# Kernel tuning notes

Measured on AMD Instinct MI355X. Metric: run time of the kernel, lower is better.

## Reference

```python
import jax, jax.numpy as jnp
import numpy as np

E, H, V, P, RAW = 512, 1024, 12000, 36, 2048
B, L = 128, 21

def setup_inputs() -> dict:
    key = jax.random.key(0)
    ks = jax.random.split(key, 16)
    n = lambda k, sh: (0.02 * jax.random.normal(k, sh)).astype(jnp.float32)
    z = lambda sh: jnp.zeros(sh, jnp.float32)
    return {
        "images_features": jax.random.normal(ks[0], (B, P, RAW), dtype=jnp.float32),
        "encoded_captions": jax.random.randint(ks[1], (B, L), 0, V),
        "caption_lengths": L,
        "W_img": n(ks[2], (RAW, H)), "b_img": z((H,)),
        "W_glob": n(ks[3], (H, E)), "b_glob": z((E,)),
        "W_ih1": n(ks[4], (2 * E + H, 4 * H)), "W_hh1": n(ks[5], (H, 4 * H)),
        "b_ih1": z((4 * H,)), "b_hh1": z((4 * H,)),
        "Wx_gate": n(ks[6], (2 * E + H, H)), "bx_gate": z((H,)),
        "Wh_gate": n(ks[7], (H, H)), "bh_gate": z((H,)),
        "W_ih2": n(ks[8], (2 * H, 4 * H)), "W_hh2": n(ks[9], (H, 4 * H)),
        "b_ih2": z((4 * H,)), "b_hh2": z((4 * H,)),
        "Wv": n(ks[10], (H, P)), "bv": z((P,)),
        "Ws": n(ks[11], (H, P)), "bs": z((P,)),
        "Wg": n(ks[12], (H, P)),
        "wh": n(ks[13], (P,)),
        "emb": n(ks[14], (V, E)),
        "W_fc": n(ks[15], (H, V)), "b_fc": z((V,)),
    }

def _lstm(x, h, c, W_ih, W_hh, b_ih, b_hh):
    # torch LSTMCell gate order: i, f, g, o
    g = x @ W_ih + b_ih + h @ W_hh + b_hh
    i, f, gg, o = jnp.split(g, 4, axis=-1)
    c_new = jax.nn.sigmoid(f) * c + jax.nn.sigmoid(i) * jnp.tanh(gg)
    h_new = jax.nn.sigmoid(o) * jnp.tanh(c_new)
    return h_new, c_new

def reference(images_features, encoded_captions, caption_lengths, W_img, b_img,
              W_glob, b_glob, W_ih1, W_hh1, b_ih1, b_hh1, Wx_gate, bx_gate,
              Wh_gate, bh_gate, W_ih2, W_hh2, b_ih2, b_hh2, Wv, bv, Ws, bs,
              Wg, wh, emb, W_fc, b_fc):
    Bsz = images_features.shape[0]
    Hd = W_hh1.shape[0]
    T = int(caption_lengths) - 1
    Vfeat = jax.nn.relu(images_features @ W_img + b_img)            # (B,P,H)
    glob = jax.nn.relu(jnp.mean(Vfeat, axis=1) @ W_glob + b_glob)   # (B,E)
    img_proj = Vfeat @ Wv + bv                                      # (B,P,P) loop-invariant
    word_embs = emb[encoded_captions[:, :T]]                        # (B,T,E)

    def step(carry, we):
        h1, c1, h2, c2 = carry
        xt = jnp.concatenate([h2, glob, we], axis=-1)               # (B, H+2E)
        h1n, c1n = _lstm(xt, h1, c1, W_ih1, W_hh1, b_ih1, b_hh1)
        sen_gate = jax.nn.sigmoid(xt @ Wx_gate + bx_gate + h1 @ Wh_gate + bh_gate)
        st = sen_gate * jnp.tanh(c1n)                               # visual sentinel
        ht_proj = h1n @ Wg                                          # (B,P)
        z = jnp.tanh(img_proj + ht_proj[:, :, None]) @ wh           # (B,P)
        alpha = jax.nn.softmax(z, axis=1)                           # (B,P)
        context = jnp.einsum('bp,bph->bh', alpha, Vfeat)            # (B,H)
        att_vs = jnp.tanh(st @ Ws + bs + ht_proj) @ wh              # (B,)
        alpha_hat = jax.nn.softmax(jnp.concatenate([z, att_vs[:, None]], axis=1), axis=1)
        beta = alpha_hat[:, -1:]                                    # (B,1)
        c_hat = beta * st + (1.0 - beta) * context
        h2n, c2n = _lstm(jnp.concatenate([c_hat, h1n], axis=-1), h2, c2,
                         W_ih2, W_hh2, b_ih2, b_hh2)
        score = (c_hat + h2n) @ W_fc + b_fc                         # (B,V)
        return (h1n, c1n, h2n, c2n), (score, alpha, beta)

    zeros = jnp.zeros((Bsz, Hd), images_features.dtype)
    init = (zeros, zeros, zeros, zeros)
    _, (preds, alphas, betas) = jax.lax.scan(step, init, jnp.swapaxes(word_embs, 0, 1))
    return (jnp.swapaxes(preds, 0, 1),   # (B,T,V)
            jnp.swapaxes(alphas, 0, 1),  # (B,T,P)
            jnp.swapaxes(betas, 0, 1))   # (B,T,1)
```

## Files before the change

kernel.cpp:

```cpp
#include <hip/hip_runtime.h>
#include <hip/hip_bf16.h>
#include <math.h>

typedef __attribute__((ext_vector_type(4))) float f32x4;
typedef __attribute__((ext_vector_type(8))) short bf16x8;

constexpr int kB = 128, kT = 20, kH = 1024, kE = 512, kP = 36, kRaw = 2048, kV = 12000;

__device__ __forceinline__ float sigf(float x) { return 1.0f / (1.0f + expf(-x)); }

#define AS1C const __attribute__((address_space(1))) void*
#define AS3P __attribute__((address_space(3))) void*

constexpr int NZ1 = 2 * kB * kH / 4;
constexpr int NZ2 = 2 * kB * kH * 2 / 16;
constexpr int NCV = kB * kP * kRaw / 4;
constexpr int NPV = 64 * 1024 * 2 / 16;
constexpr int NPF = 32 * 1024 * 2 / 16;
constexpr int NPB = 5120;
constexpr int NGE = kB * kT * kE;

__global__ __launch_bounds__(256) void prep_small(
    float* c1z, uint4* h1z, const float* images, __hip_bfloat16* imagesb,
    uint4* wtv, uint4* wtfc_pad,
    const float* b_ih1, const float* b_hh1, const float* bx, const float* bh,
    const float* b_ih2, const float* b_hh2, float* bias_g1, float* bias_g2,
    const int* caps, const float* emb, __hip_bfloat16* wembb) {
  long idx = (long)blockIdx.x * 256 + threadIdx.x;
  if (idx < NZ1) { reinterpret_cast<float4*>(c1z)[idx] = make_float4(0, 0, 0, 0); return; }
  idx -= NZ1;
  if (idx < NZ2) { h1z[idx] = make_uint4(0, 0, 0, 0); return; }
  idx -= NZ2;
  if (idx < NCV) {
    float4 v = reinterpret_cast<const float4*>(images)[idx];
    __hip_bfloat16* d = imagesb + idx * 4;
    d[0] = __float2bfloat16(v.x); d[1] = __float2bfloat16(v.y);
    d[2] = __float2bfloat16(v.z); d[3] = __float2bfloat16(v.w);
    return;
  }
  idx -= NCV;
  if (idx < NPV) { wtv[idx] = make_uint4(0, 0, 0, 0); return; }
  idx -= NPV;
  if (idx < NPF) { wtfc_pad[idx] = make_uint4(0, 0, 0, 0); return; }
  idx -= NPF;
  if (idx < NPB) {
    int i = (int)idx;
    if (i < 4096) {
      bias_g1[i] = b_ih1[i] + b_hh1[i];
      bias_g2[i] = b_ih2[i] + b_hh2[i];
    } else {
      bias_g1[i] = bx[i - 4096] + bh[i - 4096];
    }
    return;
  }
  idx -= NPB;
  if (idx < NGE) {
    int e = (int)(idx % kE);
    int bt = (int)(idx / kE);
    int t = bt % kT;
    int b = bt / kT;
    int tok = caps[b * (kT + 1) + t];
    wembb[idx] = __float2bfloat16(emb[(size_t)tok * kE + e]);
  }
}

struct TJob {
  const float* src; __hip_bfloat16* dst;
  int ld_src, K, N, lddst, koff, noff, blk_off, nbx;
};
struct TAll { TJob job[11]; int njobs; int total_blocks; };

__global__ __launch_bounds__(256) void transpose_all(TAll ta) {
  __shared__ float t[32][33];
  int bid = blockIdx.x;
  int ji = 0;
  while (ji + 1 < ta.njobs && bid >= ta.job[ji + 1].blk_off) ++ji;
  const TJob& J = ta.job[ji];
  int lbid = bid - J.blk_off;
  int n0 = (lbid % J.nbx) * 32, k0 = (lbid / J.nbx) * 32;
  int tx = threadIdx.x & 31, ty = threadIdx.x >> 5;
  #pragma unroll
  for (int i = 0; i < 32; i += 8) {
    int k = k0 + ty + i, n = n0 + tx;
    t[ty + i][tx] = (k < J.K && n < J.N) ? J.src[(size_t)k * J.ld_src + n] : 0.0f;
  }
  __syncthreads();
  #pragma unroll
  for (int i = 0; i < 32; i += 8) {
    int n = n0 + ty + i, k = k0 + tx;
    if (n < J.N && k < J.K)
      J.dst[(size_t)(n + J.noff) * J.lddst + k + J.koff] = __float2bfloat16(t[tx][ty + i]);
  }
}

struct SegB { const __hip_bfloat16* A; int lda; int kstart; int kend; };
struct GemmBArgs {
  SegB seg[4]; int nseg;
  const __hip_bfloat16* WT; int ldk;
  const float* bias;
  float* C; __hip_bfloat16* C16; int ldc; int N; int Ktot; int act; int zstride;
};

__global__ __launch_bounds__(256) void gemm_bf16(GemmBArgs ga) {
  __shared__ char lds[65536];
  const int bm = blockIdx.y * 64;
  const int bn = blockIdx.x * 64;
  const int tid = threadIdx.x;
  const int lane = tid & 63;
  const int w = tid >> 6;
  const int wr = w >> 1, wc = w & 1;

  int rowS[4], scbS[4], dstS[4];
  #pragma unroll
  for (int j = 0; j < 4; ++j) {
    int off = ((j * 4 + w) * 64 + lane) * 16;
    int row = off >> 8, colb = off & 255;
    rowS[j] = row;
    scbS[j] = colb ^ ((row & 7) << 4);
    dstS[j] = (j * 4 + w) * 1024;
  }

  f32x4 acc[2][2] = {};
  const int nz = gridDim.z;
  const int nit = (ga.Ktot >> 7) / nz;
  const int it0 = blockIdx.z * nit;
  float* C = ga.C + (size_t)blockIdx.z * ga.zstride;

  auto stage = [&](int it, int buf) {
    const int k0 = it << 7;
    int si = 0;
    while (k0 >= ga.seg[si].kend) ++si;
    const __hip_bfloat16* Aseg = ga.seg[si].A;
    const int lda = ga.seg[si].lda;
    const int ks = k0 - ga.seg[si].kstart;
    char* baseA = lds + buf * 32768;
    char* baseB = baseA + 16384;
    #pragma unroll
    for (int j = 0; j < 4; ++j) {
      const __hip_bfloat16* sA = Aseg + (size_t)(bm + rowS[j]) * lda + ks + (scbS[j] >> 1);
      __builtin_amdgcn_global_load_lds((AS1C)sA, (AS3P)(baseA + dstS[j]), 16, 0, 0);
      const __hip_bfloat16* sB = ga.WT + (size_t)(bn + rowS[j]) * ga.ldk + k0 + (scbS[j] >> 1);
      __builtin_amdgcn_global_load_lds((AS1C)sB, (AS3P)(baseB + dstS[j]), 16, 0, 0);
    }
  };

  auto compute = [&](int buf) {
    const char* baseA = lds + buf * 32768;
    const char* baseB = baseA + 16384;
    #pragma unroll
    for (int kk = 0; kk < 4; ++kk) {
      bf16x8 a[2], b[2];
      #pragma unroll
      for (int f = 0; f < 2; ++f) {
        int row = wr * 32 + f * 16 + (lane & 15);
        int cb = kk * 64 + (lane >> 4) * 16;
        a[f] = *(const bf16x8*)(baseA + row * 256 + (cb ^ ((row & 7) << 4)));
        int nl = wc * 32 + f * 16 + (lane & 15);
        b[f] = *(const bf16x8*)(baseB + nl * 256 + (cb ^ ((nl & 7) << 4)));
      }
      #pragma unroll
      for (int fm = 0; fm < 2; ++fm)
        #pragma unroll
        for (int fn = 0; fn < 2; ++fn)
          acc[fm][fn] = __builtin_amdgcn_mfma_f32_16x16x32_bf16(a[fm], b[fn], acc[fm][fn], 0, 0, 0);
    }
  };

  stage(it0, 0);
  stage(it0 + 1, 1);
  asm volatile("s_waitcnt vmcnt(8)" ::: "memory");
  __builtin_amdgcn_s_barrier();
  int cur = 0;
  for (int i = 0; i < nit; ++i) {
    compute(cur);
    __builtin_amdgcn_s_barrier();
    if (i + 2 < nit) stage(it0 + i + 2, cur);
    if (i + 1 < nit) {
      if (i + 2 < nit) asm volatile("s_waitcnt vmcnt(8)" ::: "memory");
      else             asm volatile("s_waitcnt vmcnt(0)" ::: "memory");
      __builtin_amdgcn_s_barrier();
    }
    cur ^= 1;
  }

  #pragma unroll
  for (int fm = 0; fm < 2; ++fm) {
    int rbase = bm + wr * 32 + fm * 16 + (lane >> 4) * 4;
    #pragma unroll
    for (int fn = 0; fn < 2; ++fn) {
      int col = bn + wc * 32 + fn * 16 + (lane & 15);
      if (col >= ga.N) continue;
      float bv = ga.bias ? ga.bias[col] : 0.0f;
      #pragma unroll
      for (int j = 0; j < 4; ++j) {
        float v = acc[fm][fn][j] + bv;
        if (ga.act == 1) v = fmaxf(v, 0.0f);
        size_t off = (size_t)(rbase + j) * ga.ldc + col;
        if (ga.C) C[off] = v;
        if (ga.C16) ga.C16[off] = __float2bfloat16(v);
      }
    }
  }
}

struct G128Args {
  const __hip_bfloat16* A; int lda;
  const __hip_bfloat16* WT; int ldk;
  const float* bias;
  float* C; __hip_bfloat16* C16; int ldc; int N; int Ktot; int act; int cmap;
};

__global__ __launch_bounds__(256) void gemm128(G128Args ga) {
  __shared__ char lds[65536];
  const int gx = gridDim.x;
  const int nwg = gx * gridDim.y;
  int bid = blockIdx.y * gx + blockIdx.x;
  int q = nwg >> 3, r = nwg & 7;
  int xc = bid & 7, yq = bid >> 3;
  int swz = (xc < r ? xc * (q + 1) : r * (q + 1) + (xc - r) * q) + yq;
  const int bn = (swz % gx) * 128;
  const int bm = (swz / gx) * 128;

  const int tid = threadIdx.x;
  const int lane = tid & 63;
  const int w = tid >> 6;
  const int wr = w >> 1, wc = w & 1;

  int rowS[4], scbS[4], dstS[4];
  #pragma unroll
  for (int j = 0; j < 4; ++j) {
    int off = ((j * 4 + w) * 64 + lane) * 16;
    int row = off >> 7, colb = off & 127;
    rowS[j] = row;
    scbS[j] = colb ^ ((row & 7) << 4);
    dstS[j] = (j * 4 + w) * 1024;
  }

  f32x4 acc[4][4] = {};
  const int nit = ga.Ktot >> 6;

  auto stage = [&](int it, int buf) {
    const int k0 = it << 6;
    char* baseA = lds + buf * 32768;
    char* baseB = baseA + 16384;
    #pragma unroll
    for (int j = 0; j < 4; ++j) {
      const __hip_bfloat16* sA = ga.A + (size_t)(bm + rowS[j]) * ga.lda + k0 + (scbS[j] >> 1);
      __builtin_amdgcn_global_load_lds((AS1C)sA, (AS3P)(baseA + dstS[j]), 16, 0, 0);
      const __hip_bfloat16* sB = ga.WT + (size_t)(bn + rowS[j]) * ga.ldk + k0 + (scbS[j] >> 1);
      __builtin_amdgcn_global_load_lds((AS1C)sB, (AS3P)(baseB + dstS[j]), 16, 0, 0);
    }
  };

  auto compute = [&](int buf) {
    const char* baseA = lds + buf * 32768;
    const char* baseB = baseA + 16384;
    #pragma unroll
    for (int kk = 0; kk < 2; ++kk) {
      bf16x8 a[4], b[4];
      int cb = kk * 64 + (lane >> 4) * 16;
      #pragma unroll
      for (int f = 0; f < 4; ++f) {
        int row = wr * 64 + f * 16 + (lane & 15);
        a[f] = *(const bf16x8*)(baseA + row * 128 + (cb ^ ((row & 7) << 4)));
        int nl = wc * 64 + f * 16 + (lane & 15);
        b[f] = *(const bf16x8*)(baseB + nl * 128 + (cb ^ ((nl & 7) << 4)));
      }
      #pragma unroll
      for (int fm = 0; fm < 4; ++fm)
        #pragma unroll
        for (int fn = 0; fn < 4; ++fn)
          acc[fm][fn] = __builtin_amdgcn_mfma_f32_16x16x32_bf16(a[fm], b[fn], acc[fm][fn], 0, 0, 0);
    }
  };

  stage(0, 0);
  stage(1, 1);
  asm volatile("s_waitcnt vmcnt(8)" ::: "memory");
  __builtin_amdgcn_s_barrier();
  int cur = 0;
  for (int i = 0; i < nit; ++i) {
    compute(cur);
    __builtin_amdgcn_s_barrier();
    if (i + 2 < nit) stage(i + 2, cur);
    if (i + 1 < nit) {
      if (i + 2 < nit) asm volatile("s_waitcnt vmcnt(8)" ::: "memory");
      else             asm volatile("s_waitcnt vmcnt(0)" ::: "memory");
      __builtin_amdgcn_s_barrier();
    }
    cur ^= 1;
  }

  #pragma unroll
  for (int fm = 0; fm < 4; ++fm) {
    int rbase = bm + wr * 64 + fm * 16 + (lane >> 4) * 4;
    #pragma unroll
    for (int fn = 0; fn < 4; ++fn) {
      int col = bn + wc * 64 + fn * 16 + (lane & 15);
      if (col >= ga.N) continue;
      float bv = ga.bias ? ga.bias[col] : 0.0f;
      #pragma unroll
      for (int j = 0; j < 4; ++j) {
        float v = acc[fm][fn][j] + bv;
        if (ga.act == 1) v = fmaxf(v, 0.0f);
        int m = rbase + j;
        size_t off = ga.cmap == 1
            ? (size_t)(m & 127) * ga.ldc + (size_t)(m >> 7) * kV + col
            : (size_t)m * ga.ldc + col;
        if (ga.C) ga.C[off] = v;
        if (ga.C16) ga.C16[off] = __float2bfloat16(v);
      }
    }
  }
}

__global__ __launch_bounds__(256) void mean_p(const float* __restrict__ Vfeat,
                                              __hip_bfloat16* __restrict__ meanVb) {
  int idx = blockIdx.x * 256 + threadIdx.x;
  if (idx >= kB * kH) return;
  int b = idx >> 10, h = idx & 1023;
  float sm = 0.0f;
  for (int p = 0; p < kP; ++p) sm += Vfeat[((size_t)b * kP + p) * kH + h];
  meanVb[idx] = __float2bfloat16(sm * (1.0f / kP));
}

constexpr int kSlab1 = kB * 5120;
__global__ __launch_bounds__(256) void step1_fused(
    const float* __restrict__ g, const float* __restrict__ bias_g1,
    float* __restrict__ c1, __hip_bfloat16* __restrict__ h1b,
    const float* __restrict__ img_proj, const float* __restrict__ Vfeat,
    const float* __restrict__ Wg, const float* __restrict__ Ws,
    const float* __restrict__ bs, const float* __restrict__ wh,
    float* __restrict__ c_hat, __hip_bfloat16* __restrict__ c_hatb,
    float* __restrict__ out_alphas, float* __restrict__ out_betas, int t) {
  const int b = blockIdx.x;
  const int tid = threadIdx.x;
  const int lane = tid & 63;
  const int w = tid >> 6;
  __shared__ float sh_h1[kH];
  __shared__ float sh_st[kH];
  __shared__ float wsum[4][36];
  __shared__ float htp[36];
  __shared__ float stp[36];
  __shared__ float alpha[kP];
  __shared__ float sred[4];

  const float* gr0 = g + (size_t)b * 5120;
  const float* gr1 = gr0 + kSlab1;
  #pragma unroll
  for (int i = 0; i < 4; ++i) {
    int h = tid + i * 256;
    float ig = sigf(gr0[h]           + gr1[h]           + bias_g1[h]);
    float fg = sigf(gr0[kH + h]      + gr1[kH + h]      + bias_g1[kH + h]);
    float gg = tanhf(gr0[2 * kH + h] + gr1[2 * kH + h]  + bias_g1[2 * kH + h]);
    float og = sigf(gr0[3 * kH + h]  + gr1[3 * kH + h]  + bias_g1[3 * kH + h]);
    int idx = b * kH + h;
    float c = fg * c1[idx] + ig * gg;
    float tc = tanhf(c);
    float hn = og * tc;
    c1[idx] = c;
    h1b[idx] = __float2bfloat16(hn);
    sh_h1[h] = hn;
    sh_st[h] = sigf(gr0[4 * kH + h] + gr1[4 * kH + h] + bias_g1[4 * kH + h]) * tc;
  }
  __syncthreads();

  #pragma unroll
  for (int pass = 0; pass < 2; ++pass) {
    const float* vec = pass == 0 ? sh_h1 : sh_st;
    const float* W = pass == 0 ? Wg : Ws;
    float pg[36];
    #pragma unroll
    for (int j = 0; j < 36; ++j) pg[j] = 0.0f;
    #pragma unroll
    for (int i = 0; i < 4; ++i) {
      int hh = tid + i * 256;
      float hv = vec[hh];
      const float4* wrow = reinterpret_cast<const float4*>(W + (size_t)hh * 36);
      #pragma unroll
      for (int r = 0; r < 9; ++r) {
        float4 wv = wrow[r];
        pg[4 * r + 0] = fmaf(hv, wv.x, pg[4 * r + 0]);
        pg[4 * r + 1] = fmaf(hv, wv.y, pg[4 * r + 1]);
        pg[4 * r + 2] = fmaf(hv, wv.z, pg[4 * r + 2]);
        pg[4 * r + 3] = fmaf(hv, wv.w, pg[4 * r + 3]);
      }
    }
    #pragma unroll
    for (int j = 0; j < 36; ++j) {
      float v = pg[j];
      #pragma unroll
      for (int off = 32; off > 0; off >>= 1) v += __shfl_down(v, off, 64);
      if (lane == 0) wsum[w][j] = v;
    }
    __syncthreads();
    if (tid < 36) {
      float s = wsum[0][tid] + wsum[1][tid] + wsum[2][tid] + wsum[3][tid];
      if (pass == 0) htp[tid] = s; else stp[tid] = s;
    }
    __syncthreads();
  }

  if (w == 0) {
    float zz_r = -3.0e38f;
    if (lane < kP) {
      const float* ip = img_proj + ((size_t)b * kP + lane) * kP;
      float acc = 0.0f;
      #pragma unroll
      for (int j = 0; j < kP; ++j) acc = fmaf(tanhf(ip[j] + htp[j]), wh[j], acc);
      zz_r = acc;
    }
    float m = zz_r;
    #pragma unroll
    for (int off = 32; off > 0; off >>= 1) m = fmaxf(m, __shfl_xor(m, off, 64));
    float e = (lane < kP) ? expf(zz_r - m) : 0.0f;
    float s = e;
    #pragma unroll
    for (int off = 32; off > 0; off >>= 1) s += __shfl_xor(s, off, 64);
    if (lane < kP) alpha[lane] = e / s;
    if (lane == 0) { sred[2] = m; sred[3] = s; }
  } else if (w == 1) {
    float tv = 0.0f;
    if (lane < kP) tv = tanhf(stp[lane] + bs[lane] + htp[lane]) * wh[lane];
    #pragma unroll
    for (int off = 32; off > 0; off >>= 1) tv += __shfl_xor(tv, off, 64);
    if (lane == 0) sred[0] = tv;
  }
  __syncthreads();
  if (tid == 0) {
    float av = sred[0], m = sred[2], s = sred[3];
    float m2 = fmaxf(m, av);
    float eb = expf(av - m2);
    float beta = eb / (s * expf(m - m2) + eb);
    sred[1] = beta;
    out_betas[b * kT + t] = beta;
  }
  __syncthreads();
  if (tid < kP) out_alphas[((size_t)b * kT + t) * kP + tid] = alpha[tid];
  const float beta = sred[1];
  #pragma unroll
  for (int i = 0; i < 4; ++i) {
    int h = tid + i * 256;
    float ctx = 0.0f;
    for (int p = 0; p < kP; ++p) ctx = fmaf(alpha[p], Vfeat[((size_t)b * kP + p) * kH + h], ctx);
    float v = beta * sh_st[h] + (1.0f - beta) * ctx;
    c_hat[(size_t)b * kH + h] = v;
    c_hatb[(size_t)b * kH + h] = __float2bfloat16(v);
  }
}

constexpr int kSlab2 = kB * 4096;
__global__ __launch_bounds__(256) void lstm2_elem(const float* __restrict__ g,
                                                  const float* __restrict__ bias_g2,
                                                  float* __restrict__ c2,
                                                  __hip_bfloat16* __restrict__ h2b,
                                                  const float* __restrict__ c_hat,
                                                  __hip_bfloat16* __restrict__ sbufb) {
  int idx = blockIdx.x * 256 + threadIdx.x;
  if (idx >= kB * kH) return;
  int b = idx >> 10, h = idx & 1023;
  const float* gr0 = g + (size_t)b * 4 * kH;
  const float* gr1 = gr0 + kSlab2;
  float ig = sigf(gr0[h]           + gr1[h]           + bias_g2[h]);
  float fg = sigf(gr0[kH + h]      + gr1[kH + h]      + bias_g2[kH + h]);
  float gg = tanhf(gr0[2 * kH + h] + gr1[2 * kH + h]  + bias_g2[2 * kH + h]);
  float og = sigf(gr0[3 * kH + h]  + gr1[3 * kH + h]  + bias_g2[3 * kH + h]);
  float c = fg * c2[idx] + ig * gg;
  float hn = og * tanhf(c);
  c2[idx] = c;
  h2b[idx] = __float2bfloat16(hn);
  sbufb[idx] = __float2bfloat16(c_hat[idx] + hn);
}

extern "C" void kernel_launch(void* const* d_in, const int* in_sizes, int n_in,
                              void* d_out, int out_size, void* d_ws, size_t ws_size,
                              hipStream_t stream) {
  const float* images  = (const float*)d_in[0];
  const int*   caps    = (const int*)d_in[1];
  const float* W_img   = (const float*)d_in[3];
  const float* b_img   = (const float*)d_in[4];
  const float* W_glob  = (const float*)d_in[5];
  const float* b_glob  = (const float*)d_in[6];
  const float* W_ih1   = (const float*)d_in[7];
  const float* W_hh1   = (const float*)d_in[8];
  const float* b_ih1   = (const float*)d_in[9];
  const float* b_hh1   = (const float*)d_in[10];
  const float* Wx_gate = (const float*)d_in[11];
  const float* bx_gate = (const float*)d_in[12];
  const float* Wh_gate = (const float*)d_in[13];
  const float* bh_gate = (const float*)d_in[14];
  const float* W_ih2   = (const float*)d_in[15];
  const float* W_hh2   = (const float*)d_in[16];
  const float* b_ih2   = (const float*)d_in[17];
  const float* b_hh2   = (const float*)d_in[18];
  const float* Wv      = (const float*)d_in[19];
  const float* bv      = (const float*)d_in[20];
  const float* Ws_     = (const float*)d_in[21];
  const float* bs_     = (const float*)d_in[22];
  const float* Wg      = (const float*)d_in[23];
  const float* wh      = (const float*)d_in[24];
  const float* emb     = (const float*)d_in[25];
  const float* W_fc    = (const float*)d_in[26];
  const float* b_fc    = (const float*)d_in[27];

  float* out = (float*)d_out;
  float* out_alphas = out + (size_t)kB * kT * kV;
  float* out_betas  = out_alphas + (size_t)kB * kT * kP;

  char* base = (char*)d_ws;
  auto alloc = [&](size_t bytes) {
    char* p = base;
    base += (bytes + 255) & ~(size_t)255;
    return p;
  };
  float*          Vfeat   = (float*)alloc((size_t)kB * kP * kH * 4);
  __hip_bfloat16* Vfeatb  = (__hip_bfloat16*)alloc((size_t)kB * kP * kH * 2);
  __hip_bfloat16* imagesb = (__hip_bfloat16*)alloc((size_t)kB * kP * kRaw * 2);
  __hip_bfloat16* WTg1    = (__hip_bfloat16*)alloc((size_t)5120 * 3072 * 2);
  __hip_bfloat16* WTg2    = (__hip_bfloat16*)alloc((size_t)4096 * 3072 * 2);
  __hip_bfloat16* WTfc    = (__hip_bfloat16*)alloc((size_t)12032 * 1024 * 2);
  __hip_bfloat16* WTimg   = (__hip_bfloat16*)alloc((size_t)1024 * 2048 * 2);
  __hip_bfloat16* WTglob  = (__hip_bfloat16*)alloc((size_t)512 * 1024 * 2);
  __hip_bfloat16* WTv     = (__hip_bfloat16*)alloc((size_t)64 * 1024 * 2);
  __hip_bfloat16* wembb   = (__hip_bfloat16*)alloc((size_t)kB * kT * kE * 2);
  float*          img_proj= (float*)alloc((size_t)kB * kP * kP * 4);
  __hip_bfloat16* globb   = (__hip_bfloat16*)alloc((size_t)kB * kE * 2);
  __hip_bfloat16* meanVb  = (__hip_bfloat16*)alloc((size_t)kB * kH * 2);
  float*          c1      = (float*)alloc((size_t)2 * kB * kH * 4);
  float*          c2      = c1 + kB * kH;
  __hip_bfloat16* h1b     = (__hip_bfloat16*)alloc((size_t)2 * kB * kH * 2);
  __hip_bfloat16* h2b     = h1b + kB * kH;
  float*          g1out   = (float*)alloc((size_t)2 * kB * 5120 * 4);
  float*          chat    = (float*)alloc((size_t)kB * kH * 4);
  __hip_bfloat16* chatb   = (__hip_bfloat16*)alloc((size_t)kB * kH * 2);
  __hip_bfloat16* sbufall = (__hip_bfloat16*)alloc((size_t)kT * kB * kH * 2);
  float*          bias_g1 = (float*)alloc(5120 * 4);
  float*          bias_g2 = (float*)alloc(4096 * 4);

  {
    long total = (long)NZ1 + NZ2 + NCV + NPV + NPF + NPB + NGE;
    int blocks = (int)((total + 255) / 256);
    prep_small<<<blocks, 256, 0, stream>>>(
        c1, (uint4*)h1b, images, imagesb, (uint4*)WTv,
        (uint4*)(WTfc + (size_t)12000 * 1024),
        b_ih1, b_hh1, bx_gate, bh_gate, b_ih2, b_hh2, bias_g1, bias_g2,
        caps, emb, wembb);
  }
  {
    TAll ta = {};
    int off = 0, j = 0;
    auto add = [&](const float* src, int ldsrc, int K, int N, __hip_bfloat16* dst,
                   int lddst, int koff, int noff) {
      int nbx = (N + 31) / 32, nby = (K + 31) / 32;
      ta.job[j] = {src, dst, ldsrc, K, N, lddst, koff, noff, off, nbx};
      off += nbx * nby;
      ++j;
    };
    add(W_img,   kH,     kRaw, kH,     WTimg,  kRaw, 0, 0);
    add(W_glob,  kE,     kH,   kE,     WTglob, kH,   0, 0);
    add(Wv,      kP,     kH,   kP,     WTv,    kH,   0, 0);
    add(W_ih1,   4 * kH, 2048, 4 * kH, WTg1,   3072, 0, 0);
    add(W_hh1,   4 * kH, 1024, 4 * kH, WTg1,   3072, 2048, 0);
    add(Wx_gate, kH,     2048, kH,     WTg1,   3072, 0, 4096);
    add(Wh_gate, kH,     1024, kH,     WTg1,   3072, 2048, 4096);
    add(W_ih2,   4 * kH, 2048, 4 * kH, WTg2,   3072, 0, 0);
    add(W_hh2,   4 * kH, 1024, 4 * kH, WTg2,   3072, 2048, 0);
    add(W_fc,    kV,     kH,   kV,     WTfc,   kH,   0, 0);
    ta.njobs = j;
    ta.total_blocks = off;
    transpose_all<<<off, 256, 0, stream>>>(ta);
  }

  {
    G128Args ga = {};
    ga.A = imagesb; ga.lda = kRaw; ga.WT = WTimg; ga.ldk = kRaw; ga.bias = b_img;
    ga.C = Vfeat; ga.C16 = Vfeatb; ga.ldc = kH; ga.N = kH; ga.Ktot = kRaw;
    ga.act = 1; ga.cmap = 0;
    gemm128<<<dim3(kH / 128, kB * kP / 128), 256, 0, stream>>>(ga);
  }
  mean_p<<<(kB * kH + 255) / 256, 256, 0, stream>>>(Vfeat, meanVb);
  {
    GemmBArgs ga = {};
    ga.seg[0] = {meanVb, kH, 0, kH};
    ga.nseg = 1; ga.WT = WTglob; ga.ldk = kH; ga.bias = b_glob;
    ga.C = nullptr; ga.C16 = globb; ga.ldc = kE; ga.N = kE; ga.Ktot = kH; ga.act = 1;
    gemm_bf16<<<dim3(kE / 64, kB / 64, 1), 256, 0, stream>>>(ga);
  }
  {
    GemmBArgs ga = {};
    ga.seg[0] = {Vfeatb, kH, 0, kH};
    ga.nseg = 1; ga.WT = WTv; ga.ldk = kH; ga.bias = bv;
    ga.C = img_proj; ga.C16 = nullptr; ga.ldc = kP; ga.N = kP; ga.Ktot = kH; ga.act = 0;
    gemm_bf16<<<dim3(1, kB * kP / 64, 1), 256, 0, stream>>>(ga);
  }

  for (int t = 0; t < kT; ++t) {
    {
      GemmBArgs ga = {};
      ga.seg[0] = {h2b, kH, 0, kH};
      ga.seg[1] = {globb, kE, kH, kH + kE};
      ga.seg[2] = {wembb + (size_t)t * kE, kT * kE, kH + kE, 2048};
      ga.seg[3] = {h1b, kH, 2048, 3072};
      ga.nseg = 4; ga.WT = WTg1; ga.ldk = 3072; ga.bias = nullptr;
      ga.C = g1out; ga.C16 = nullptr; ga.ldc = 5120; ga.N = 5120; ga.Ktot = 3072;
      ga.act = 0; ga.zstride = kSlab1;
      gemm_bf16<<<dim3(5120 / 64, kB / 64, 2), 256, 0, stream>>>(ga);
    }
    step1_fused<<<kB, 256, 0, stream>>>(g1out, bias_g1, c1, h1b, img_proj, Vfeat,
                                        Wg, Ws_, bs_, wh, chat, chatb,
                                        out_alphas, out_betas, t);
    {
      GemmBArgs ga = {};
      ga.seg[0] = {chatb, kH, 0, kH};
      ga.seg[1] = {h1b, kH, kH, 2048};
      ga.seg[2] = {h2b, kH, 2048, 3072};
      ga.nseg = 3; ga.WT = WTg2; ga.ldk = 3072; ga.bias = nullptr;
      ga.C = g1out; ga.C16 = nullptr; ga.ldc = 4096; ga.N = 4096; ga.Ktot = 3072;
      ga.act = 0; ga.zstride = kSlab2;
      gemm_bf16<<<dim3(4096 / 64, kB / 64, 2), 256, 0, stream>>>(ga);
    }
    lstm2_elem<<<(kB * kH + 255) / 256, 256, 0, stream>>>(
        g1out, bias_g2, c2, h2b, chat, sbufall + (size_t)t * kB * kH);
  }

  {
    G128Args ga = {};
    ga.A = sbufall; ga.lda = kH; ga.WT = WTfc; ga.ldk = kH; ga.bias = b_fc;
    ga.C = out; ga.C16 = nullptr; ga.ldc = kT * kV; ga.N = kV; ga.Ktot = kH;
    ga.act = 0; ga.cmap = 1;
    gemm128<<<dim3(12032 / 128, kT * kB / 128), 256, 0, stream>>>(ga);
  }
}
```

Baseline: 1.588 ms.

## Hoist loop-invariant glob/word-embedding gate projections out of the recurrent loop

```diff
diff --git a/kernel.cpp b/kernel.cpp
--- a/kernel.cpp
+++ b/kernel.cpp
@@ -64,11 +64,25 @@
   }
 }
 
+__global__ __launch_bounds__(256) void build_astat(const __hip_bfloat16* __restrict__ globb,
+                                                   const __hip_bfloat16* __restrict__ wembb,
+                                                   uint4* __restrict__ astat) {
+  int idx = blockIdx.x * 256 + threadIdx.x;
+  if (idx >= kT * kB * 1024 / 8) return;
+  int m = idx >> 7;
+  int c = (idx & 127) * 8;
+  int b = m & 127, t = m >> 7;
+  const __hip_bfloat16* src = (c < 512)
+      ? globb + b * 512 + c
+      : wembb + ((size_t)(b * kT + t)) * 512 + (c - 512);
+  astat[idx] = *reinterpret_cast<const uint4*>(src);
+}
+
 struct TJob {
   const float* src; __hip_bfloat16* dst;
   int ld_src, K, N, lddst, koff, noff, blk_off, nbx;
 };
-struct TAll { TJob job[11]; int njobs; int total_blocks; };
+struct TAll { TJob job[12]; int njobs; int total_blocks; };
 
 __global__ __launch_bounds__(256) void transpose_all(TAll ta) {
   __shared__ float t[32][33];
@@ -207,19 +221,21 @@
   const __hip_bfloat16* A; int lda;
   const __hip_bfloat16* WT; int ldk;
   const float* bias;
-  float* C; __hip_bfloat16* C16; int ldc; int N; int Ktot; int act; int cmap;
+  float* C; __hip_bfloat16* C16; int ldc; int N; int Ktot; int act; int cmap; int morder;
 };
 
 __global__ __launch_bounds__(256) void gemm128(G128Args ga) {
   __shared__ char lds[65536];
   const int gx = gridDim.x;
-  const int nwg = gx * gridDim.y;
+  const int gy = gridDim.y;
+  const int nwg = gx * gy;
   int bid = blockIdx.y * gx + blockIdx.x;
   int q = nwg >> 3, r = nwg & 7;
   int xc = bid & 7, yq = bid >> 3;
   int swz = (xc < r ? xc * (q + 1) : r * (q + 1) + (xc - r) * q) + yq;
-  const int bn = (swz % gx) * 128;
-  const int bm = (swz / gx) * 128;
+  int bn, bm;
+  if (ga.morder == 1) { bm = (swz % gy) * 128; bn = (swz / gy) * 128; }
+  else                { bn = (swz % gx) * 128; bm = (swz / gx) * 128; }
 
   const int tid = threadIdx.x;
   const int lane = tid & 63;
@@ -326,7 +342,7 @@
 
 constexpr int kSlab1 = kB * 5120;
 __global__ __launch_bounds__(256) void step1_fused(
-    const float* __restrict__ g, const float* __restrict__ bias_g1,
+    const float* __restrict__ g, const float* __restrict__ gstat,
     float* __restrict__ c1, __hip_bfloat16* __restrict__ h1b,
     const float* __restrict__ img_proj, const float* __restrict__ Vfeat,
     const float* __restrict__ Wg, const float* __restrict__ Ws,
@@ -347,13 +363,14 @@
 
   const float* gr0 = g + (size_t)b * 5120;
   const float* gr1 = gr0 + kSlab1;
+  const float* gs  = gstat + ((size_t)t * kB + b) * 5120;
   #pragma unroll
   for (int i = 0; i < 4; ++i) {
     int h = tid + i * 256;
-    float ig = sigf(gr0[h]           + gr1[h]           + bias_g1[h]);
-    float fg = sigf(gr0[kH + h]      + gr1[kH + h]      + bias_g1[kH + h]);
-    float gg = tanhf(gr0[2 * kH + h] + gr1[2 * kH + h]  + bias_g1[2 * kH + h]);
-    float og = sigf(gr0[3 * kH + h]  + gr1[3 * kH + h]  + bias_g1[3 * kH + h]);
+    float ig = sigf(gr0[h]           + gr1[h]           + gs[h]);
+    float fg = sigf(gr0[kH + h]      + gr1[kH + h]      + gs[kH + h]);
+    float gg = tanhf(gr0[2 * kH + h] + gr1[2 * kH + h]  + gs[2 * kH + h]);
+    float og = sigf(gr0[3 * kH + h]  + gr1[3 * kH + h]  + gs[3 * kH + h]);
     int idx = b * kH + h;
     float c = fg * c1[idx] + ig * gg;
     float tc = tanhf(c);
@@ -361,7 +378,7 @@
     c1[idx] = c;
     h1b[idx] = __float2bfloat16(hn);
     sh_h1[h] = hn;
-    sh_st[h] = sigf(gr0[4 * kH + h] + gr1[4 * kH + h] + bias_g1[4 * kH + h]) * tc;
+    sh_st[h] = sigf(gr0[4 * kH + h] + gr1[4 * kH + h] + gs[4 * kH + h]) * tc;
   }
   __syncthreads();
 
@@ -516,7 +533,8 @@
   float*          Vfeat   = (float*)alloc((size_t)kB * kP * kH * 4);
   __hip_bfloat16* Vfeatb  = (__hip_bfloat16*)alloc((size_t)kB * kP * kH * 2);
   __hip_bfloat16* imagesb = (__hip_bfloat16*)alloc((size_t)kB * kP * kRaw * 2);
-  __hip_bfloat16* WTg1    = (__hip_bfloat16*)alloc((size_t)5120 * 3072 * 2);
+  __hip_bfloat16* WTg1d   = (__hip_bfloat16*)alloc((size_t)5120 * 2048 * 2);
+  __hip_bfloat16* WTg1s   = (__hip_bfloat16*)alloc((size_t)5120 * 1024 * 2);
   __hip_bfloat16* WTg2    = (__hip_bfloat16*)alloc((size_t)4096 * 3072 * 2);
   __hip_bfloat16* WTfc    = (__hip_bfloat16*)alloc((size_t)12032 * 1024 * 2);
   __hip_bfloat16* WTimg   = (__hip_bfloat16*)alloc((size_t)1024 * 2048 * 2);
@@ -534,6 +552,8 @@
   float*          chat    = (float*)alloc((size_t)kB * kH * 4);
   __hip_bfloat16* chatb   = (__hip_bfloat16*)alloc((size_t)kB * kH * 2);
   __hip_bfloat16* sbufall = (__hip_bfloat16*)alloc((size_t)kT * kB * kH * 2);
+  __hip_bfloat16* Astat   = (__hip_bfloat16*)alloc((size_t)kT * kB * 1024 * 2);
+  float*          g1stat  = (float*)alloc((size_t)kT * kB * 5120 * 4);
   float*          bias_g1 = (float*)alloc(5120 * 4);
   float*          bias_g2 = (float*)alloc(4096 * 4);
 
@@ -559,10 +579,12 @@
     add(W_img,   kH,     kRaw, kH,     WTimg,  kRaw, 0, 0);
     add(W_glob,  kE,     kH,   kE,     WTglob, kH,   0, 0);
     add(Wv,      kP,     kH,   kP,     WTv,    kH,   0, 0);
-    add(W_ih1,   4 * kH, 2048, 4 * kH, WTg1,   3072, 0, 0);
-    add(W_hh1,   4 * kH, 1024, 4 * kH, WTg1,   3072, 2048, 0);
-    add(Wx_gate, kH,     2048, kH,     WTg1,   3072, 0, 4096);
-    add(Wh_gate, kH,     1024, kH,     WTg1,   3072, 2048, 4096);
+    add(W_ih1,   4 * kH, 1024, 4 * kH, WTg1d,  2048, 0, 0);
+    add(W_hh1,   4 * kH, 1024, 4 * kH, WTg1d,  2048, 1024, 0);
+    add(Wx_gate, kH,     1024, kH,     WTg1d,  2048, 0, 4096);
+    add(Wh_gate, kH,     1024, kH,     WTg1d,  2048, 1024, 4096);
+    add(W_ih1 + (size_t)1024 * 4 * kH, 4 * kH, 1024, 4 * kH, WTg1s, 1024, 0, 0);
+    add(Wx_gate + (size_t)1024 * kH,   kH,     1024, kH,     WTg1s, 1024, 0, 4096);
     add(W_ih2,   4 * kH, 2048, 4 * kH, WTg2,   3072, 0, 0);
     add(W_hh2,   4 * kH, 1024, 4 * kH, WTg2,   3072, 2048, 0);
     add(W_fc,    kV,     kH,   kV,     WTfc,   kH,   0, 0);
@@ -575,7 +597,7 @@
     G128Args ga = {};
     ga.A = imagesb; ga.lda = kRaw; ga.WT = WTimg; ga.ldk = kRaw; ga.bias = b_img;
     ga.C = Vfeat; ga.C16 = Vfeatb; ga.ldc = kH; ga.N = kH; ga.Ktot = kRaw;
-    ga.act = 1; ga.cmap = 0;
+    ga.act = 1; ga.cmap = 0; ga.morder = 0;
     gemm128<<<dim3(kH / 128, kB * kP / 128), 256, 0, stream>>>(ga);
   }
   mean_p<<<(kB * kH + 255) / 256, 256, 0, stream>>>(Vfeat, meanVb);
@@ -586,6 +608,15 @@
     ga.C = nullptr; ga.C16 = globb; ga.ldc = kE; ga.N = kE; ga.Ktot = kH; ga.act = 1;
     gemm_bf16<<<dim3(kE / 64, kB / 64, 1), 256, 0, stream>>>(ga);
   }
+  build_astat<<<(kT * kB * 1024 / 8 + 255) / 256, 256, 0, stream>>>(globb, wembb,
+                                                                    (uint4*)Astat);
+  {
+    G128Args ga = {};
+    ga.A = Astat; ga.lda = 1024; ga.WT = WTg1s; ga.ldk = 1024; ga.bias = bias_g1;
+    ga.C = g1stat; ga.C16 = nullptr; ga.ldc = 5120; ga.N = 5120; ga.Ktot = 1024;
+    ga.act = 0; ga.cmap = 0; ga.morder = 1;
+    gemm128<<<dim3(5120 / 128, kT * kB / 128), 256, 0, stream>>>(ga);
+  }
   {
     GemmBArgs ga = {};
     ga.seg[0] = {Vfeatb, kH, 0, kH};
@@ -598,15 +629,13 @@
     {
       GemmBArgs ga = {};
       ga.seg[0] = {h2b, kH, 0, kH};
-      ga.seg[1] = {globb, kE, kH, kH + kE};
-      ga.seg[2] = {wembb + (size_t)t * kE, kT * kE, kH + kE, 2048};
-      ga.seg[3] = {h1b, kH, 2048, 3072};
-      ga.nseg = 4; ga.WT = WTg1; ga.ldk = 3072; ga.bias = nullptr;
-      ga.C = g1out; ga.C16 = nullptr; ga.ldc = 5120; ga.N = 5120; ga.Ktot = 3072;
+      ga.seg[1] = {h1b, kH, kH, 2048};
+      ga.nseg = 2; ga.WT = WTg1d; ga.ldk = 2048; ga.bias = nullptr;
+      ga.C = g1out; ga.C16 = nullptr; ga.ldc = 5120; ga.N = 5120; ga.Ktot = 2048;
       ga.act = 0; ga.zstride = kSlab1;
       gemm_bf16<<<dim3(5120 / 64, kB / 64, 2), 256, 0, stream>>>(ga);
     }
-    step1_fused<<<kB, 256, 0, stream>>>(g1out, bias_g1, c1, h1b, img_proj, Vfeat,
+    step1_fused<<<kB, 256, 0, stream>>>(g1out, g1stat, c1, h1b, img_proj, Vfeat,
                                         Wg, Ws_, bs_, wh, chat, chatb,
                                         out_alphas, out_betas, t);
     {
@@ -627,7 +656,7 @@
     G128Args ga = {};
     ga.A = sbufall; ga.lda = kH; ga.WT = WTfc; ga.ldk = kH; ga.bias = b_fc;
     ga.C = out; ga.C16 = nullptr; ga.ldc = kT * kV; ga.N = kV; ga.Ktot = kH;
-    ga.act = 0; ga.cmap = 1;
+    ga.act = 0; ga.cmap = 1; ga.morder = 1;
     gemm128<<<dim3(12032 / 128, kT * kB / 128), 256, 0, stream>>>(ga);
   }
 }
```

Result: no change. 1.585 ms (-0.2%).

## Split recurrent GEMMs three ways over K and retune final FC GEMM tiling

Applied to the files above, without the earlier changes.

```diff
diff --git a/kernel.cpp b/kernel.cpp
--- a/kernel.cpp
+++ b/kernel.cpp
@@ -6,6 +6,8 @@
 typedef __attribute__((ext_vector_type(8))) short bf16x8;
 
 constexpr int kB = 128, kT = 20, kH = 1024, kE = 512, kP = 36, kRaw = 2048, kV = 12000;
+constexpr int kSlab1 = kB * 5120;
+constexpr int kSlab2 = kB * 4096;
 
 __device__ __forceinline__ float sigf(float x) { return 1.0f / (1.0f + expf(-x)); }
 
@@ -68,7 +70,7 @@
   const float* src; __hip_bfloat16* dst;
   int ld_src, K, N, lddst, koff, noff, blk_off, nbx;
 };
-struct TAll { TJob job[11]; int njobs; int total_blocks; };
+struct TAll { TJob job[12]; int njobs; int total_blocks; };
 
 __global__ __launch_bounds__(256) void transpose_all(TAll ta) {
   __shared__ float t[32][33];
@@ -207,44 +209,51 @@
   const __hip_bfloat16* A; int lda;
   const __hip_bfloat16* WT; int ldk;
   const float* bias;
-  float* C; __hip_bfloat16* C16; int ldc; int N; int Ktot; int act; int cmap;
+  float* C; __hip_bfloat16* C16; int ldc; int N; int Ktot; int act; int cmap; int morder;
 };
 
+template <int BK>
 __global__ __launch_bounds__(256) void gemm128(G128Args ga) {
-  __shared__ char lds[65536];
+  constexpr int RB = BK * 2;
+  constexpr int TILEB = 128 * RB;
+  constexpr int ROUNDS = TILEB / 4096;
+  constexpr int SWZ = (RB == 256) ? 15 : (RB == 128 ? 7 : 3);
+  __shared__ char lds[2 * 2 * TILEB];
   const int gx = gridDim.x;
-  const int nwg = gx * gridDim.y;
+  const int gy = gridDim.y;
+  const int nwg = gx * gy;
   int bid = blockIdx.y * gx + blockIdx.x;
   int q = nwg >> 3, r = nwg & 7;
   int xc = bid & 7, yq = bid >> 3;
   int swz = (xc < r ? xc * (q + 1) : r * (q + 1) + (xc - r) * q) + yq;
-  const int bn = (swz % gx) * 128;
-  const int bm = (swz / gx) * 128;
+  int bn, bm;
+  if (ga.morder == 1) { bm = (swz % gy) * 128; bn = (swz / gy) * 128; }
+  else                { bn = (swz % gx) * 128; bm = (swz / gx) * 128; }
 
   const int tid = threadIdx.x;
   const int lane = tid & 63;
   const int w = tid >> 6;
   const int wr = w >> 1, wc = w & 1;
 
-  int rowS[4], scbS[4], dstS[4];
-  #pragma unroll
-  for (int j = 0; j < 4; ++j) {
+  int rowS[ROUNDS], scbS[ROUNDS], dstS[ROUNDS];
+  #pragma unroll
+  for (int j = 0; j < ROUNDS; ++j) {
     int off = ((j * 4 + w) * 64 + lane) * 16;
-    int row = off >> 7, colb = off & 127;
+    int row = off / RB, colb = off % RB;
     rowS[j] = row;
-    scbS[j] = colb ^ ((row & 7) << 4);
-    dstS[j] = (j * 4 + w) * 1024;
+    scbS[j] = colb ^ ((row & SWZ) << 4);
+    dstS[j] = off;
   }
 
   f32x4 acc[4][4] = {};
-  const int nit = ga.Ktot >> 6;
+  const int nit = ga.Ktot / BK;
 
   auto stage = [&](int it, int buf) {
-    const int k0 = it << 6;
-    char* baseA = lds + buf * 32768;
-    char* baseB = baseA + 16384;
-    #pragma unroll
-    for (int j = 0; j < 4; ++j) {
+    const int k0 = it * BK;
+    char* baseA = lds + buf * 2 * TILEB;
+    char* baseB = baseA + TILEB;
+    #pragma unroll
+    for (int j = 0; j < ROUNDS; ++j) {
       const __hip_bfloat16* sA = ga.A + (size_t)(bm + rowS[j]) * ga.lda + k0 + (scbS[j] >> 1);
       __builtin_amdgcn_global_load_lds((AS1C)sA, (AS3P)(baseA + dstS[j]), 16, 0, 0);
       const __hip_bfloat16* sB = ga.WT + (size_t)(bn + rowS[j]) * ga.ldk + k0 + (scbS[j] >> 1);
@@ -253,18 +262,18 @@
   };
 
   auto compute = [&](int buf) {
-    const char* baseA = lds + buf * 32768;
-    const char* baseB = baseA + 16384;
-    #pragma unroll
-    for (int kk = 0; kk < 2; ++kk) {
+    const char* baseA = lds + buf * 2 * TILEB;
+    const char* baseB = baseA + TILEB;
+    #pragma unroll
+    for (int kk = 0; kk < BK / 32; ++kk) {
       bf16x8 a[4], b[4];
       int cb = kk * 64 + (lane >> 4) * 16;
       #pragma unroll
       for (int f = 0; f < 4; ++f) {
         int row = wr * 64 + f * 16 + (lane & 15);
-        a[f] = *(const bf16x8*)(baseA + row * 128 + (cb ^ ((row & 7) << 4)));
+        a[f] = *(const bf16x8*)(baseA + row * RB + (cb ^ ((row & SWZ) << 4)));
         int nl = wc * 64 + f * 16 + (lane & 15);
-        b[f] = *(const bf16x8*)(baseB + nl * 128 + (cb ^ ((nl & 7) << 4)));
+        b[f] = *(const bf16x8*)(baseB + nl * RB + (cb ^ ((nl & SWZ) << 4)));
       }
       #pragma unroll
       for (int fm = 0; fm < 4; ++fm)
@@ -274,9 +283,14 @@
     }
   };
 
+  auto wait_one_stage = [&]() {
+    if constexpr (ROUNDS == 4) asm volatile("s_waitcnt vmcnt(8)" ::: "memory");
+    else                       asm volatile("s_waitcnt vmcnt(4)" ::: "memory");
+  };
+
   stage(0, 0);
   stage(1, 1);
-  asm volatile("s_waitcnt vmcnt(8)" ::: "memory");
+  wait_one_stage();
   __builtin_amdgcn_s_barrier();
   int cur = 0;
   for (int i = 0; i < nit; ++i) {
@@ -284,7 +298,7 @@
     __builtin_amdgcn_s_barrier();
     if (i + 2 < nit) stage(i + 2, cur);
     if (i + 1 < nit) {
-      if (i + 2 < nit) asm volatile("s_waitcnt vmcnt(8)" ::: "memory");
+      if (i + 2 < nit) wait_one_stage();
       else             asm volatile("s_waitcnt vmcnt(0)" ::: "memory");
       __builtin_amdgcn_s_barrier();
     }
@@ -324,7 +338,6 @@
   meanVb[idx] = __float2bfloat16(sm * (1.0f / kP));
 }
 
-constexpr int kSlab1 = kB * 5120;
 __global__ __launch_bounds__(256) void step1_fused(
     const float* __restrict__ g, const float* __restrict__ bias_g1,
     float* __restrict__ c1, __hip_bfloat16* __restrict__ h1b,
@@ -347,13 +360,14 @@
 
   const float* gr0 = g + (size_t)b * 5120;
   const float* gr1 = gr0 + kSlab1;
+  const float* gr2 = gr1 + kSlab1;
   #pragma unroll
   for (int i = 0; i < 4; ++i) {
     int h = tid + i * 256;
-    float ig = sigf(gr0[h]           + gr1[h]           + bias_g1[h]);
-    float fg = sigf(gr0[kH + h]      + gr1[kH + h]      + bias_g1[kH + h]);
-    float gg = tanhf(gr0[2 * kH + h] + gr1[2 * kH + h]  + bias_g1[2 * kH + h]);
-    float og = sigf(gr0[3 * kH + h]  + gr1[3 * kH + h]  + bias_g1[3 * kH + h]);
+    float ig = sigf(gr0[h]           + gr1[h]           + gr2[h]           + bias_g1[h]);
+    float fg = sigf(gr0[kH + h]      + gr1[kH + h]      + gr2[kH + h]      + bias_g1[kH + h]);
+    float gg = tanhf(gr0[2 * kH + h] + gr1[2 * kH + h]  + gr2[2 * kH + h]  + bias_g1[2 * kH + h]);
+    float og = sigf(gr0[3 * kH + h]  + gr1[3 * kH + h]  + gr2[3 * kH + h]  + bias_g1[3 * kH + h]);
     int idx = b * kH + h;
     float c = fg * c1[idx] + ig * gg;
     float tc = tanhf(c);
@@ -361,7 +375,7 @@
     c1[idx] = c;
     h1b[idx] = __float2bfloat16(hn);
     sh_h1[h] = hn;
-    sh_st[h] = sigf(gr0[4 * kH + h] + gr1[4 * kH + h] + bias_g1[4 * kH + h]) * tc;
+    sh_st[h] = sigf(gr0[4 * kH + h] + gr1[4 * kH + h] + gr2[4 * kH + h] + bias_g1[4 * kH + h]) * tc;
   }
   __syncthreads();
 
@@ -449,7 +463,6 @@
   }
 }
 
-constexpr int kSlab2 = kB * 4096;
 __global__ __launch_bounds__(256) void lstm2_elem(const float* __restrict__ g,
                                                   const float* __restrict__ bias_g2,
                                                   float* __restrict__ c2,
@@ -461,10 +474,11 @@
   int b = idx >> 10, h = idx & 1023;
   const float* gr0 = g + (size_t)b * 4 * kH;
   const float* gr1 = gr0 + kSlab2;
-  float ig = sigf(gr0[h]           + gr1[h]           + bias_g2[h]);
-  float fg = sigf(gr0[kH + h]      + gr1[kH + h]      + bias_g2[kH + h]);
-  float gg = tanhf(gr0[2 * kH + h] + gr1[2 * kH + h]  + bias_g2[2 * kH + h]);
-  float og = sigf(gr0[3 * kH + h]  + gr1[3 * kH + h]  + bias_g2[3 * kH + h]);
+  const float* gr2 = gr1 + kSlab2;
+  float ig = sigf(gr0[h]           + gr1[h]           + gr2[h]           + bias_g2[h]);
+  float fg = sigf(gr0[kH + h]      + gr1[kH + h]      + gr2[kH + h]      + bias_g2[kH + h]);
+  float gg = tanhf(gr0[2 * kH + h] + gr1[2 * kH + h]  + gr2[2 * kH + h]  + bias_g2[2 * kH + h]);
+  float og = sigf(gr0[3 * kH + h]  + gr1[3 * kH + h]  + gr2[3 * kH + h]  + bias_g2[3 * kH + h]);
   float c = fg * c2[idx] + ig * gg;
   float hn = og * tanhf(c);
   c2[idx] = c;
@@ -530,7 +544,7 @@
   float*          c2      = c1 + kB * kH;
   __hip_bfloat16* h1b     = (__hip_bfloat16*)alloc((size_t)2 * kB * kH * 2);
   __hip_bfloat16* h2b     = h1b + kB * kH;
-  float*          g1out   = (float*)alloc((size_t)2 * kB * 5120 * 4);
+  float*          g1out   = (float*)alloc((size_t)3 * kB * 5120 * 4);
   float*          chat    = (float*)alloc((size_t)kB * kH * 4);
   __hip_bfloat16* chatb   = (__hip_bfloat16*)alloc((size_t)kB * kH * 2);
   __hip_bfloat16* sbufall = (__hip_bfloat16*)alloc((size_t)kT * kB * kH * 2);
@@ -575,8 +589,8 @@
     G128Args ga = {};
     ga.A = imagesb; ga.lda = kRaw; ga.WT = WTimg; ga.ldk = kRaw; ga.bias = b_img;
     ga.C = Vfeat; ga.C16 = Vfeatb; ga.ldc = kH; ga.N = kH; ga.Ktot = kRaw;
-    ga.act = 1; ga.cmap = 0;
-    gemm128<<<dim3(kH / 128, kB * kP / 128), 256, 0, stream>>>(ga);
+    ga.act = 1; ga.cmap = 0; ga.morder = 0;
+    gemm128<64><<<dim3(kH / 128, kB * kP / 128), 256, 0, stream>>>(ga);
   }
   mean_p<<<(kB * kH + 255) / 256, 256, 0, stream>>>(Vfeat, meanVb);
   {
@@ -604,7 +618,7 @@
       ga.nseg = 4; ga.WT = WTg1; ga.ldk = 3072; ga.bias = nullptr;
       ga.C = g1out; ga.C16 = nullptr; ga.ldc = 5120; ga.N = 5120; ga.Ktot = 3072;
       ga.act = 0; ga.zstride = kSlab1;
-      gemm_bf16<<<dim3(5120 / 64, kB / 64, 2), 256, 0, stream>>>(ga);
+      gemm_bf16<<<dim3(5120 / 64, kB / 64, 3), 256, 0, stream>>>(ga);
     }
     step1_fused<<<kB, 256, 0, stream>>>(g1out, bias_g1, c1, h1b, img_proj, Vfeat,
                                         Wg, Ws_, bs_, wh, chat, chatb,
@@ -617,7 +631,7 @@
       ga.nseg = 3; ga.WT = WTg2; ga.ldk = 3072; ga.bias = nullptr;
       ga.C = g1out; ga.C16 = nullptr; ga.ldc = 4096; ga.N = 4096; ga.Ktot = 3072;
       ga.act = 0; ga.zstride = kSlab2;
-      gemm_bf16<<<dim3(4096 / 64, kB / 64, 2), 256, 0, stream>>>(ga);
+      gemm_bf16<<<dim3(4096 / 64, kB / 64, 3), 256, 0, stream>>>(ga);
     }
     lstm2_elem<<<(kB * kH + 255) / 256, 256, 0, stream>>>(
         g1out, bias_g2, c2, h2b, chat, sbufall + (size_t)t * kB * kH);
@@ -627,7 +641,7 @@
     G128Args ga = {};
     ga.A = sbufall; ga.lda = kH; ga.WT = WTfc; ga.ldk = kH; ga.bias = b_fc;
     ga.C = out; ga.C16 = nullptr; ga.ldc = kT * kV; ga.N = kV; ga.Ktot = kH;
-    ga.act = 0; ga.cmap = 1;
-    gemm128<<<dim3(12032 / 128, kT * kB / 128), 256, 0, stream>>>(ga);
-  }
-}
+    ga.act = 0; ga.cmap = 1; ga.morder = 1;
+    gemm128<32><<<dim3(12032 / 128, kT * kB / 128), 256, 0, stream>>>(ga);
+  }
+}
```

Result: faster. 1.537 ms (-3.2%).
